# Optimization experiments

Hardware: AMD Instinct MI355X
Metric: run time of the kernel (lower is better)

## Reference

```python
import jax, jax.numpy as jnp
import numpy as np

EPS = 1e-5

def _inorm(x, gamma=None, beta=None):
    # InstanceNorm1d: normalize over last (length) axis per (batch, channel)
    mu = jnp.mean(x, axis=-1, keepdims=True)
    var = jnp.mean(jnp.square(x - mu), axis=-1, keepdims=True)
    y = (x - mu) * jax.lax.rsqrt(var + EPS)
    if gamma is not None:
        y = y * gamma[None, :, None] + beta[None, :, None]
    return y

def _conv1x1(w, x):
    # Conv1d kernel-size-1, bias=False -> channel GEMM
    return jnp.einsum('oi,bin->bon', w, x)

def _channel_attn(Q, K, V, scale):
    scores = jnp.einsum('bin,bjn->bij', Q, K) * scale  # [B, qc, kc]
    attn = jax.nn.softmax(_inorm(scores), axis=-1)
    return jnp.einsum('bij,bjn->bin', attn, V)


def setup_inputs() -> dict:
    key = jax.random.key(0)
    ks = jax.random.split(key, 12)
    C, EC, NC, N = 256, 256, 2, 16384
    H = W = 128
    twoB = 8
    s = C ** -0.5
    return {
        'features': jax.random.normal(ks[0], (twoB, C, H, W), jnp.float32),
        'kv_queue': jax.random.normal(ks[1], (NC, EC, N), jnp.float32) * 0.01,
        'w_in': jax.random.normal(ks[2], (EC, C), jnp.float32) * s,
        'w_out': jax.random.normal(ks[3], (C, EC), jnp.float32) * s,
        'wq_sa': jax.random.normal(ks[4], (EC, EC), jnp.float32) * s,
        'wk_sa': jax.random.normal(ks[5], (EC, EC), jnp.float32) * s,
        'wv_sa': jax.random.normal(ks[6], (EC, EC), jnp.float32) * s,
        'wo_sa': jax.random.normal(ks[7], (EC, EC), jnp.float32) * s,
        'wq_ca': jax.random.normal(ks[8], (EC, EC), jnp.float32) * s,
        'wo_ca': jax.random.normal(ks[9], (EC, EC), jnp.float32) * s,
        'attn_gamma': jnp.ones((EC,), jnp.float32),
        'attn_beta': jnp.zeros((EC,), jnp.float32),
        'enc_gamma': jnp.ones((EC,), jnp.float32),
        'enc_beta': jnp.zeros((EC,), jnp.float32),
    }


def reference(features, kv_queue, w_in, w_out, wq_sa, wk_sa, wv_sa, wo_sa,
              wq_ca, wo_ca, attn_gamma, attn_beta, enc_gamma, enc_beta):
    twoB, C, H, W = features.shape
    B = twoB // 2
    N = H * W
    scale = N ** -0.5
    x = features.reshape(twoB, C, N)
    # map_in: 1x1 conv + exact GELU
    emb = jax.nn.gelu(_conv1x1(w_in, x), approximate=False)
    emb_l, emb_u = emb[:B], emb[B:]
    norm = _inorm(emb, attn_gamma, attn_beta)  # per-sample, safe to batch both halves
    norm_l, norm_u = norm[:B], norm[B:]
    # --- self-attention on unlabeled half (channel-wise) ---
    Qu = _conv1x1(wq_sa, norm_u)
    Ku = _conv1x1(wk_sa, norm_u)
    Vu = _conv1x1(wv_sa, norm_u)
    sa_u = _conv1x1(wo_sa, _channel_attn(Qu, Ku, Vu, scale)) + emb_u
    # --- cross-attention: labeled queries vs semantic-memory queue ---
    Ql = _conv1x1(wq_ca, norm_l)  # [B, ec, N]
    nc, ec, Nq = kv_queue.shape
    kv = kv_queue.reshape(nc * ec, Nq)  # [num_class*ec, N], shared across batch
    scores = jnp.einsum('bin,jn->bij', Ql, kv) * scale  # [B, ec, nc*ec]
    attn = jax.nn.softmax(_inorm(scores), axis=-1)
    ca = jnp.einsum('bij,jn->bin', attn, kv)
    ca_l = _conv1x1(wo_ca, ca) + emb_l
    # --- map_out on enc-normed halves ---
    out_l = jax.nn.gelu(_conv1x1(w_out, _inorm(ca_l, enc_gamma, enc_beta)), approximate=False)
    out_u = jax.nn.gelu(_conv1x1(w_out, _inorm(sa_u, enc_gamma, enc_beta)), approximate=False)
    out = jnp.concatenate([out_l, out_u], axis=0)
    return out.reshape(twoB, C, H, W)
```

## Files before the change

### kernel.cpp

```cpp
#include <hip/hip_runtime.h>
#include <hip/hip_bf16.h>

#define N_DIM 16384
#define CN (256L * 16384)
#define NT_Q 8
#define NT_KCH (N_DIM / NT_Q)

using bf16 = __hip_bfloat16;

typedef __attribute__((ext_vector_type(8))) short short8;
typedef __attribute__((ext_vector_type(4))) float f32x4;
typedef __attribute__((ext_vector_type(4))) unsigned int u32x4;


__device__ __forceinline__ unsigned short f2bf(float x) {
    unsigned int u = __float_as_uint(x);
    u = (u + 0x7FFFu + ((u >> 16) & 1u)) >> 16;
    return (unsigned short)u;
}
__device__ __forceinline__ float bfus2f(unsigned short h) {
    return __uint_as_float(((unsigned int)h) << 16);
}

__device__ __forceinline__ void mfma16(f32x4& d, short8 a, short8 b) {
    asm("v_mfma_f32_16x16x32_bf16 %0, %1, %2, %0" : "+v"(d) : "v"(a), "v"(b));
}

__device__ inline float ldmix(const void* p, long i, int isbf) {
    return isbf ? __bfloat162float(((const bf16*)p)[i])
                : ((const float*)p)[i];
}

__device__ inline void st_out(float* p, long i, float v)  { p[i] = v; }
__device__ inline void st_out(bf16* p, long i, float v)   { p[i] = __float2bfloat16(v); }

__device__ inline float gelu_f(float x) {
    return 0.5f * x * (1.0f + erff(x * 0.70710678118654752440f));
}

__device__ inline float block_reduce_sum(float v, float* sh) {
    int t = threadIdx.x;
    sh[t] = v; __syncthreads();
    for (int s = 128; s >= 1; s >>= 1) {
        if (t < s) sh[t] += sh[t + s];
        __syncthreads();
    }
    float r = sh[0]; __syncthreads();
    return r;
}

__device__ inline float block_reduce_max(float v, float* sh) {
    int t = threadIdx.x;
    sh[t] = v; __syncthreads();
    for (int s = 128; s >= 1; s >>= 1) {
        if (t < s) sh[t] = fmaxf(sh[t], sh[t + s]);
        __syncthreads();
    }
    float r = sh[0]; __syncthreads();
    return r;
}

__device__ __forceinline__ void wr16(short* d, const u32x4* r, int isbf) {
    if (isbf) {
        *(u32x4*)d = r[0]; *(u32x4*)(d + 8) = r[1];
    } else {
        #pragma unroll
        for (int g = 0; g < 2; ++g) {
            short8 h;
            #pragma unroll
            for (int i = 0; i < 8; ++i)
                h[i] = (short)f2bf(__uint_as_float(r[2*g + (i >> 2)][i & 3]));
            *(short8*)(d + g * 8) = h;
        }
    }
}


__global__ void detect_main(const unsigned short* __restrict__ p, int* __restrict__ flag) {
    __shared__ int cnt;
    int t = threadIdx.x;
    if (t == 0) cnt = 0;
    __syncthreads();
    int e = (p[t] >> 7) & 0xFF;
    if (e >= 90 && e <= 145) atomicAdd(&cnt, 1);
    __syncthreads();
    if (t == 0) *flag = (cnt >= 200) ? 1 : 0;
}

__global__ void detect_const(const unsigned short* __restrict__ p, int* __restrict__ flag) {
    __shared__ int zc;
    int t = threadIdx.x;
    if (t == 0) zc = 0;
    __syncthreads();
    if (p[t] == 0) atomicAdd(&zc, 1);
    __syncthreads();
    if (t == 0) *flag = (zc >= 64) ? 0 : 1;
}

__global__ void init_consts(int* flags) {
    flags[2] = 0;
    flags[3] = 1;
}

__global__ void cvt_small(const void* __restrict__ in, float* __restrict__ out,
                          int n, const int* __restrict__ flag) {
    int i = threadIdx.x;
    if (i < n) out[i] = ldmix(in, i, *flag);
}

__global__ void rowsum_kv(const void* __restrict__ kv, float* __restrict__ kvsum,
                          const int* __restrict__ flag) {
    __shared__ float sh[256];
    int j = blockIdx.x, t = threadIdx.x, isbf = *flag;
    float s = 0.f;
    if (isbf) {
        const short8* p = (const short8*)((const bf16*)kv + (long)j * N_DIM);
        for (int i = t; i < N_DIM / 8; i += 256) {
            short8 v = p[i];
            #pragma unroll
            for (int e = 0; e < 8; ++e) s += bfus2f((unsigned short)v[e]);
        }
    } else {
        const float4* p = (const float4*)((const float*)kv + (long)j * N_DIM);
        for (int i = t; i < N_DIM / 4; i += 256) {
            float4 v = p[i];
            s += v.x + v.y + v.z + v.w;
        }
    }
    s = block_reduce_sum(s, sh);
    if (t == 0) kvsum[j] = s;
}

__global__ void row_stats(const bf16* __restrict__ Z,
                          const float* __restrict__ gamma,
                          const float* __restrict__ beta,
                          float4* __restrict__ st) {
    __shared__ float sh[256];
    int row = blockIdx.x, z = blockIdx.y, t = threadIdx.x;
    const short8* zp = (const short8*)(Z + (long)z * CN + (long)row * N_DIM);
    float s = 0.f, s2 = 0.f;
    for (int i = t; i < N_DIM / 8; i += 256) {
        short8 v = zp[i];
        #pragma unroll
        for (int e = 0; e < 8; ++e) {
            float x = bfus2f((unsigned short)v[e]);
            s += x; s2 += x * x;
        }
    }
    float sum  = block_reduce_sum(s, sh);
    float sum2 = block_reduce_sum(s2, sh);
    if (t == 0) {
        float mean = sum * (1.0f / N_DIM);
        float var  = fmaxf(sum2 * (1.0f / N_DIM) - mean * mean, 0.0f);
        float inv  = rsqrtf(var + 1e-5f);
        float sc = gamma[row] * inv;
        st[z * 256 + row] = make_float4(sc, beta[row] - mean * sc, mean, 0.0f);
    }
}

__global__ void inorm_softmax(float* __restrict__ S, int L) {
    __shared__ float sh[256];
    float* row = S + (long)blockIdx.x * L;
    int t = threadIdx.x;
    float x0 = row[t];
    float x1 = (L > 256) ? row[t + 256] : 0.0f;
    float sum = block_reduce_sum(x0 + x1, sh);
    float mean = sum / (float)L;
    float d0 = x0 - mean;
    float d1 = (L > 256) ? (x1 - mean) : 0.0f;
    float var = fmaxf(block_reduce_sum(d0 * d0 + d1 * d1, sh) / (float)L, 0.0f);
    float inv = rsqrtf(var + 1e-5f);
    float y0 = d0 * inv, y1 = d1 * inv;
    float mx = (L > 256) ? fmaxf(y0, y1) : y0;
    float gmax = block_reduce_max(mx, sh);
    float e0 = expf(y0 - gmax);
    float e1 = (L > 256) ? expf(y1 - gmax) : 0.0f;
    float es = block_reduce_sum(e0 + e1, sh);
    float rinv = 1.0f / es;
    row[t] = e0 * rinv;
    if (L > 256) row[t + 256] = e1 * rinv;
}

template <bool RES, bool GELU, typename TOUT>
__global__ __launch_bounds__(256) void gemm_nn_mfma(
    const void* __restrict__ Ag, const int* __restrict__ fA, long astr,
    const void* __restrict__ Bg, const int* __restrict__ fB, long bbase, long bstr,
    const float* __restrict__ rowc, int rstr,
    const bf16* __restrict__ Dres, long dstr,
    TOUT* __restrict__ Cout, long cstr, int K)
{
    __shared__ short Ahi[2][128 * 40];
    __shared__ short Alo[2][128 * 40];
    __shared__ short Bsm[2][32 * 130];

    int t = threadIdx.x;
    int af = *fA, bfg = *fB;
    int z = blockIdx.z;
    int n0 = blockIdx.x * 128, m0 = blockIdx.y * 128;
    int wave = t >> 6, lane = t & 63;
    int wr = wave >> 1, wc = wave & 1;
    int l15 = lane & 15, lkg = lane >> 4;
    int arow = t & 127, ah2 = t >> 7;

    long abase = (long)z * astr;
    long bz = bbase + (long)z * bstr;

    u32x4 ra[4], rb[4];
    f32x4 acc[4][4];
    f32x4 zz = {0.f, 0.f, 0.f, 0.f};
    #pragma unroll
    for (int mi = 0; mi < 4; ++mi)
        #pragma unroll
        for (int ni = 0; ni < 4; ++ni) acc[mi][ni] = zz;

    auto STAGE_LOAD = [&](int k0) {
        long ga = abase + (long)(m0 + arow) * K + k0 + ah2 * 16;
        if (af) {
            const u32x4* p = (const u32x4*)((const unsigned short*)Ag + ga);
            ra[0] = p[0]; ra[1] = p[1];
        } else {
            const u32x4* p = (const u32x4*)((const float*)Ag + ga);
            ra[0] = p[0]; ra[1] = p[1]; ra[2] = p[2]; ra[3] = p[3];
        }
        #pragma unroll
        for (int c = 0; c < 2; ++c) {
            int q = c * 256 + t;
            int k = q >> 4, n = (q & 15) * 8;
            long gb = bz + (long)(k0 + k) * N_DIM + n0 + n;
            if (bfg) {
                rb[c * 2] = *(const u32x4*)((const unsigned short*)Bg + gb);
            } else {
                const u32x4* p = (const u32x4*)((const float*)Bg + gb);
                rb[c * 2] = p[0]; rb[c * 2 + 1] = p[1];
            }
        }
    };

    auto STAGE_WRITE = [&](int b2) {
        short* dh = &Ahi[b2][arow * 40 + ah2 * 16];
        short* dl = &Alo[b2][arow * 40 + ah2 * 16];
        if (af) {
            *(u32x4*)dh = ra[0]; *(u32x4*)(dh + 8) = ra[1];
            u32x4 z4 = {0u, 0u, 0u, 0u};
            *(u32x4*)dl = z4; *(u32x4*)(dl + 8) = z4;
        } else {
            #pragma unroll
            for (int g = 0; g < 2; ++g) {
                short8 h, l;
                #pragma unroll
                for (int i = 0; i < 8; ++i) {
                    float x = __uint_as_float(ra[2 * g + (i >> 2)][i & 3]);
                    unsigned short hu = f2bf(x);
                    h[i] = (short)hu;
                    l[i] = (short)f2bf(x - bfus2f(hu));
                }
                *(short8*)(dh + g * 8) = h;
                *(short8*)(dl + g * 8) = l;
            }
        }
        #pragma unroll
        for (int c = 0; c < 2; ++c) {
            int q = c * 256 + t;
            int k = q >> 4, n = (q & 15) * 8;
            unsigned int* wp = (unsigned int*)&Bsm[b2][k * 130 + n];
            if (bfg) {
                const unsigned int* s = (const unsigned int*)&rb[c * 2];
                wp[0] = s[0]; wp[1] = s[1]; wp[2] = s[2]; wp[3] = s[3];
            } else {
                #pragma unroll
                for (int j = 0; j < 4; ++j) {
                    float x0 = __uint_as_float(rb[c * 2 + (j >> 1)][(j & 1) * 2]);
                    float x1 = __uint_as_float(rb[c * 2 + (j >> 1)][(j & 1) * 2 + 1]);
                    wp[j] = (unsigned int)f2bf(x0) | ((unsigned int)f2bf(x1) << 16);
                }
            }
        }
    };

    auto COMPUTE = [&](int b2) {
        const short* AhB = &Ahi[b2][0];
        const short* AlB = &Alo[b2][0];
        const short* BsB = &Bsm[b2][0];
        short8 bfr[4];
        #pragma unroll
        for (int ni = 0; ni < 4; ++ni) {
            short8 v;
            #pragma unroll
            for (int e = 0; e < 8; ++e)
                v[e] = BsB[(lkg * 8 + e) * 130 + wc * 64 + ni * 16 + l15];
            bfr[ni] = v;
        }
        short8 ahf[4], alf[4];
        #pragma unroll
        for (int mi = 0; mi < 4; ++mi) {
            int ro = (wr * 64 + mi * 16 + l15) * 40 + lkg * 8;
            ahf[mi] = *(const short8*)(AhB + ro);
            alf[mi] = *(const short8*)(AlB + ro);
        }
        #pragma unroll
        for (int mi = 0; mi < 4; ++mi)
            #pragma unroll
            for (int ni = 0; ni < 4; ++ni)
                mfma16(acc[mi][ni], ahf[mi], bfr[ni]);
        #pragma unroll
        for (int mi = 0; mi < 4; ++mi)
            #pragma unroll
            for (int ni = 0; ni < 4; ++ni)
                mfma16(acc[mi][ni], alf[mi], bfr[ni]);
    };

    int nsteps = K >> 5;
    STAGE_LOAD(0);
    STAGE_WRITE(0);
    __syncthreads();
    int buf = 0;
    for (int s = 0; s < nsteps; ++s) {
        bool pre = (s + 1 < nsteps);
        if (pre) STAGE_LOAD((s + 1) << 5);
        COMPUTE(buf);
        if (pre) STAGE_WRITE(buf ^ 1);
        __syncthreads();
        buf ^= 1;
    }

    long cz = (long)z * cstr;
    long dz = (long)z * dstr;
    #pragma unroll
    for (int mi = 0; mi < 4; ++mi) {
        #pragma unroll
        for (int ni = 0; ni < 4; ++ni) {
            int mbase = m0 + wr * 64 + mi * 16 + lkg * 4;
            int n = n0 + wc * 64 + ni * 16 + l15;
            #pragma unroll
            for (int r = 0; r < 4; ++r) {
                int m = mbase + r;
                float v = acc[mi][ni][r];
                if (rowc) v += rowc[z * rstr + m];
                if (RES)  v += __bfloat162float(Dres[dz + (long)m * N_DIM + n]);
                if (GELU) v = gelu_f(v);
                st_out(Cout, cz + (long)m * N_DIM + n, v);
            }
        }
    }
}

__global__ __launch_bounds__(256) void gemm_nt_mfma(
    const void* __restrict__ Ag, const int* __restrict__ fA, long astr,
    const void* __restrict__ Bg, const int* __restrict__ fB, long bstr,
    float* __restrict__ Pout, int J)
{
    __shared__ short Ash[2][128 * 40];
    __shared__ short Bs2[2][128 * 40];

    int t = threadIdx.x;
    int af = *fA, bfg = *fB;
    int zq = blockIdx.z;
    int zb = zq >> 3, q = zq & 7;
    int j0 = blockIdx.x * 128, m0 = blockIdx.y * 128;
    int kz = q * NT_KCH;
    int wave = t >> 6, lane = t & 63;
    int wr = wave >> 1, wc = wave & 1;
    int l15 = lane & 15, lkg = lane >> 4;
    int arow = t & 127, ah2 = t >> 7;

    long abase = (long)zb * astr;
    long bbase = (long)zb * bstr;

    u32x4 ra[4], rbn[4];
    f32x4 acc[4][4];
    f32x4 zz = {0.f, 0.f, 0.f, 0.f};
    #pragma unroll
    for (int mi = 0; mi < 4; ++mi)
        #pragma unroll
        for (int nj = 0; nj < 4; ++nj) acc[mi][nj] = zz;

    auto STAGE_LOAD = [&](int k0) {
        long ga = abase + (long)(m0 + arow) * N_DIM + k0 + ah2 * 16;
        if (af) {
            const u32x4* p = (const u32x4*)((const unsigned short*)Ag + ga);
            ra[0] = p[0]; ra[1] = p[1];
        } else {
            const u32x4* p = (const u32x4*)((const float*)Ag + ga);
            ra[0] = p[0]; ra[1] = p[1]; ra[2] = p[2]; ra[3] = p[3];
        }
        long gb = bbase + (long)(j0 + arow) * N_DIM + k0 + ah2 * 16;
        if (bfg) {
            const u32x4* p = (const u32x4*)((const unsigned short*)Bg + gb);
            rbn[0] = p[0]; rbn[1] = p[1];
        } else {
            const u32x4* p = (const u32x4*)((const float*)Bg + gb);
            rbn[0] = p[0]; rbn[1] = p[1]; rbn[2] = p[2]; rbn[3] = p[3];
        }
    };

    auto STAGE_WRITE = [&](int b2) {
        wr16(&Ash[b2][arow * 40 + ah2 * 16], ra, af);
        wr16(&Bs2[b2][arow * 40 + ah2 * 16], rbn, bfg);
    };

    auto COMPUTE = [&](int b2) {
        const short* AsB = &Ash[b2][0];
        const short* BsB = &Bs2[b2][0];
        short8 a[4], b[4];
        #pragma unroll
        for (int mi = 0; mi < 4; ++mi)
            a[mi] = *(const short8*)(AsB + (wr * 64 + mi * 16 + l15) * 40 + lkg * 8);
        #pragma unroll
        for (int nj = 0; nj < 4; ++nj)
            b[nj] = *(const short8*)(BsB + (wc * 64 + nj * 16 + l15) * 40 + lkg * 8);
        #pragma unroll
        for (int mi = 0; mi < 4; ++mi)
            #pragma unroll
            for (int nj = 0; nj < 4; ++nj)
                mfma16(acc[mi][nj], a[mi], b[nj]);
    };

    int nsteps = NT_KCH >> 5;
    STAGE_LOAD(kz);
    STAGE_WRITE(0);
    __syncthreads();
    int buf = 0;
    for (int s = 0; s < nsteps; ++s) {
        bool pre = (s + 1 < nsteps);
        if (pre) STAGE_LOAD(kz + ((s + 1) << 5));
        COMPUTE(buf);
        if (pre) STAGE_WRITE(buf ^ 1);
        __syncthreads();
        buf ^= 1;
    }

    float* P = Pout + (long)zq * 256 * J;
    #pragma unroll
    for (int mi = 0; mi < 4; ++mi) {
        #pragma unroll
        for (int nj = 0; nj < 4; ++nj) {
            int mbase = m0 + wr * 64 + mi * 16 + lkg * 4;
            int j = j0 + wc * 64 + nj * 16 + l15;
            #pragma unroll
            for (int r = 0; r < 4; ++r)
                P[(long)(mbase + r) * J + j] = acc[mi][nj][r];
        }
    }
}

template <bool TRANSB>
__global__ __launch_bounds__(256) void gemm_small(
    const void* __restrict__ A, const int* __restrict__ fA, int K, long astr,
    const void* __restrict__ B, const int* __restrict__ fB, int ldb, long bstr,
    float* __restrict__ C, int Nn, long cstr, float alpha)
{
    __shared__ float As[64][65];
    __shared__ float Bs[64][65];
    int af = *fA, bfg = *fB;
    int z = blockIdx.z;
    int j0 = blockIdx.x * 64, m0 = blockIdx.y * 64;
    int t = threadIdx.x, tx = t & 15, ty = t >> 4;
    long ab = (long)z * astr, bb = (long)z * bstr;
    float acc[4][4] = {{0.f}};

    for (int k0 = 0; k0 < K; k0 += 64) {
        #pragma unroll
        for (int i = 0; i < 16; ++i) {
            int idx = t + i * 256;
            int r = idx >> 6, c = idx & 63;
            As[c][r] = ldmix(A, ab + (long)(m0 + r) * K + (k0 + c), af);
            if (TRANSB)
                Bs[c][r] = ldmix(B, bb + (long)(j0 + r) * ldb + (k0 + c), bfg);
            else
                Bs[r][c] = ldmix(B, bb + (long)(k0 + r) * ldb + (j0 + c), bfg);
        }
        __syncthreads();
        #pragma unroll
        for (int kk = 0; kk < 64; ++kk) {
            float a[4], bbv[4];
            #pragma unroll
            for (int i = 0; i < 4; ++i) a[i] = As[kk][ty * 4 + i];
            #pragma unroll
            for (int j = 0; j < 4; ++j) bbv[j] = Bs[kk][tx * 4 + j];
            #pragma unroll
            for (int i = 0; i < 4; ++i)
                #pragma unroll
                for (int j = 0; j < 4; ++j)
                    acc[i][j] = fmaf(a[i], bbv[j], acc[i][j]);
        }
        __syncthreads();
    }

    #pragma unroll
    for (int i = 0; i < 4; ++i) {
        int m = m0 + ty * 4 + i;
        #pragma unroll
        for (int j = 0; j < 4; ++j)
            C[(long)z * cstr + (long)m * Nn + (j0 + tx * 4 + j)] = acc[i][j] * alpha;
    }
}


__global__ void build_G(const float* __restrict__ PART, const float4* __restrict__ st,
                        float* __restrict__ G) {
    int z = blockIdx.y, c = blockIdx.x, d = threadIdx.x;
    float g = 0.f;
    for (int q = 0; q < NT_Q; ++q)
        g += PART[((long)(z * NT_Q + q)) * 65536 + c * 256 + d];
    float4 a = st[z * 256 + c], b = st[z * 256 + d];
    float rc = a.z * (float)N_DIM, rd = b.z * (float)N_DIM;
    G[(long)z * 65536 + c * 256 + d] = a.x * b.x * g
                   + a.x * b.y * rc + a.y * b.x * rd
                   + (float)N_DIM * a.y * b.y;
}

__global__ void build_P(const float* __restrict__ PART, const float4* __restrict__ st,
                        const float* __restrict__ kvsum, float* __restrict__ P) {
    int z = blockIdx.y, c = blockIdx.x, t = threadIdx.x;
    float4 a = st[z * 256 + c];
    for (int j = t; j < 512; j += 256) {
        float s = 0.f;
        for (int q = 0; q < NT_Q; ++q)
            s += PART[((long)(z * NT_Q + q)) * 131072 + c * 512 + j];
        P[(long)z * 131072 + c * 512 + j] = a.x * s + a.y * kvsum[j];
    }
}

__global__ void build_Ms_u(const float* __restrict__ M, const float4* __restrict__ st,
                           float* __restrict__ Ms, float* __restrict__ u) {
    __shared__ float sh[256];
    int z = blockIdx.y, m = blockIdx.x, c = threadIdx.x;
    float mv = M[(long)z * 65536 + m * 256 + c];
    float4 b = st[z * 256 + c];
    Ms[(long)z * 65536 + m * 256 + c] = mv * b.x + ((m == c) ? 1.0f : 0.0f);
    float uu = block_reduce_sum(mv * b.y, sh);
    if (c == 0) u[z * 256 + m] = uu;
}

__global__ void build_W2_v(const void* __restrict__ Wout, const int* __restrict__ fM,
                           const float4* __restrict__ st,
                           float* __restrict__ W2, float* __restrict__ v) {
    __shared__ float sh[256];
    int z = blockIdx.y, o = blockIdx.x, c = threadIdx.x;
    float wv = ldmix(Wout, (long)o * 256 + c, *fM);
    float4 b = st[z * 256 + c];
    W2[(long)z * 65536 + o * 256 + c] = wv * b.x;
    float vv = block_reduce_sum(wv * b.y, sh);
    if (c == 0) v[z * 256 + o] = vv;
}

extern "C" void kernel_launch(void* const* d_in, const int* in_sizes, int n_in,
                              void* d_out, int out_size, void* d_ws, size_t ws_size,
                              hipStream_t stream) {
    const void* feats = d_in[0];
    const void* kv    = d_in[1];
    const void* W_in  = d_in[2];
    const void* W_out = d_in[3];
    const void* Wq_sa = d_in[4];
    const void* Wk_sa = d_in[5];
    const void* Wv_sa = d_in[6];
    const void* Wo_sa = d_in[7];
    const void* Wq_ca = d_in[8];
    const void* Wo_ca = d_in[9];
    float* OUT = (float*)d_out;

    char* w = (char*)d_ws;
    auto alloc = [&](size_t bytes) { char* p = w; w += (bytes + 255) & ~255UL; return p; };
    int*    flags = (int*)alloc(64);
    float*  GA    = (float*)alloc(1024);
    float*  GAb   = (float*)alloc(1024);
    float*  EG    = (float*)alloc(1024);
    float*  EGb   = (float*)alloc(1024);
    float*  kvsum = (float*)alloc(2048);
    float4* ST1   = (float4*)alloc(8 * 256 * 16);
    float4* ST2   = (float4*)alloc(8 * 256 * 16);
    float*  Gf4   = (float*)alloc(4L * 65536 * 4);
    float*  T1_4  = (float*)alloc(4L * 65536 * 4);
    float*  T2_4  = (float*)alloc(4L * 65536 * 4);
    float*  Mm4   = (float*)alloc(4L * 65536 * 4);
    float*  Ms4   = (float*)alloc(4L * 65536 * 4);
    float*  W2_8  = (float*)alloc(8L * 65536 * 4);
    float*  SC4   = (float*)alloc(4L * 65536 * 4);
    float*  SCL4  = (float*)alloc(4L * 131072 * 4);
    float*  Pm4   = (float*)alloc(4L * 131072 * 4);
    float*  M2_4  = (float*)alloc(4L * 131072 * 4);
    float*  uvec  = (float*)alloc(4 * 256 * 4);
    float*  vvec  = (float*)alloc(8 * 256 * 4);
    float*  PART  = (float*)alloc(32L * 131072 * 4);
    bf16*   EMB8  = (bf16*)alloc(8 * CN * 2);
    bf16*   SU8   = (bf16*)alloc(8 * CN * 2);

    const int* fM = flags + 0;
    const int* f0 = flags + 2;
    const int* f1 = flags + 3;
    const float scale = 1.0f / 128.0f;

    detect_main<<<1, 256, 0, stream>>>((const unsigned short*)feats, flags + 0);
    detect_const<<<1, 256, 0, stream>>>((const unsigned short*)d_in[10], flags + 1);
    init_consts<<<1, 1, 0, stream>>>(flags);
    cvt_small<<<1, 256, 0, stream>>>(d_in[10], GA,  256, flags + 1);
    cvt_small<<<1, 256, 0, stream>>>(d_in[11], GAb, 256, flags + 1);
    cvt_small<<<1, 256, 0, stream>>>(d_in[12], EG,  256, flags + 1);
    cvt_small<<<1, 256, 0, stream>>>(d_in[13], EGb, 256, flags + 1);
    rowsum_kv<<<512, 256, 0, stream>>>(kv, kvsum, fM);

    gemm_nn_mfma<false, true, bf16><<<dim3(128, 2, 8), 256, 0, stream>>>(
        W_in, fM, 0, feats, fM, 0, CN, nullptr, 0, nullptr, 0, EMB8, CN, 256);
    row_stats<<<dim3(256, 8), 256, 0, stream>>>(EMB8, GA, GAb, ST1);

    gemm_nt_mfma<<<dim3(2, 2, 32), 256, 0, stream>>>(
        EMB8 + 4 * CN, f1, CN, EMB8 + 4 * CN, f1, CN, PART, 256);
    build_G<<<dim3(256, 4), 256, 0, stream>>>(PART, ST1 + 4 * 256, Gf4);
    gemm_small<false><<<dim3(4, 4, 4), 256, 0, stream>>>(
        Wq_sa, fM, 256, 0, Gf4, f0, 256, 65536, T1_4, 256, 65536, 1.0f);
    gemm_small<true><<<dim3(4, 4, 4), 256, 0, stream>>>(
        T1_4, f0, 256, 65536, Wk_sa, fM, 256, 0, SC4, 256, 65536, scale);
    inorm_softmax<<<1024, 256, 0, stream>>>(SC4, 256);
    gemm_small<false><<<dim3(4, 4, 4), 256, 0, stream>>>(
        Wo_sa, fM, 256, 0, SC4, f0, 256, 65536, T2_4, 256, 65536, 1.0f);
    gemm_small<false><<<dim3(4, 4, 4), 256, 0, stream>>>(
        T2_4, f0, 256, 65536, Wv_sa, fM, 256, 0, Mm4, 256, 65536, 1.0f);
    build_Ms_u<<<dim3(256, 4), 256, 0, stream>>>(Mm4, ST1 + 4 * 256, Ms4, uvec);
    gemm_nn_mfma<false, false, bf16><<<dim3(128, 2, 4), 256, 0, stream>>>(
        Ms4, f0, 65536, EMB8, f1, 4 * CN, CN, uvec, 256, nullptr, 0, SU8 + 4 * CN, CN, 256);

    gemm_nt_mfma<<<dim3(4, 2, 32), 256, 0, stream>>>(
        EMB8, f1, CN, kv, fM, 0, PART, 512);
    build_P<<<dim3(256, 4), 256, 0, stream>>>(PART, ST1, kvsum, Pm4);
    gemm_small<false><<<dim3(8, 4, 4), 256, 0, stream>>>(
        Wq_ca, fM, 256, 0, Pm4, f0, 512, 131072, SCL4, 512, 131072, scale);
    inorm_softmax<<<1024, 256, 0, stream>>>(SCL4, 512);
    gemm_small<false><<<dim3(8, 4, 4), 256, 0, stream>>>(
        Wo_ca, fM, 256, 0, SCL4, f0, 512, 131072, M2_4, 512, 131072, 1.0f);
    gemm_nn_mfma<true, false, bf16><<<dim3(128, 2, 4), 256, 0, stream>>>(
        M2_4, f0, 131072, kv, fM, 0, 0, nullptr, 0, EMB8, CN, SU8, CN, 512);

    row_stats<<<dim3(256, 8), 256, 0, stream>>>(SU8, EG, EGb, ST2);
    build_W2_v<<<dim3(256, 8), 256, 0, stream>>>(W_out, fM, ST2, W2_8, vvec);
    gemm_nn_mfma<false, true, float><<<dim3(128, 2, 8), 256, 0, stream>>>(
        W2_8, f0, 65536, SU8, f1, 0, CN, vvec, 256, nullptr, 0, OUT, CN, 256);
}
```

Before: 1.458 ms.

## Transpose B tile into K-contiguous LDS layout and skip lo-MFMA for bf16 A

The B operand is now loaded as strided column pairs and transposed while being written to LDS, so each MFMA B fragment becomes a single vector read instead of eight scalar LDS reads. When A is already bf16, the kernel no longer zero-fills the low-part A buffer and skips the second MFMA pass that previously multiplied by zeros. The cost is that B global loads become narrower and strided across rows (4-byte or 8-byte per row), which may hurt coalescing.

Result: no change. 1.476 ms (+1.2%).

```diff
diff --git a/kernel.cpp b/kernel.cpp
--- a/kernel.cpp
+++ b/kernel.cpp
@@ -191,7 +191,7 @@
 {
     __shared__ short Ahi[2][128 * 40];
     __shared__ short Alo[2][128 * 40];
-    __shared__ short Bsm[2][32 * 130];
+    __shared__ short Bt [2][128 * 40];
 
     int t = threadIdx.x;
     int af = *fA, bfg = *fB;
@@ -201,11 +201,13 @@
     int wr = wave >> 1, wc = wave & 1;
     int l15 = lane & 15, lkg = lane >> 4;
     int arow = t & 127, ah2 = t >> 7;
+    int kq = t & 7, npl = t >> 3;
 
     long abase = (long)z * astr;
     long bz = bbase + (long)z * bstr;
 
-    u32x4 ra[4], rb[4];
+    u32x4 ra[4];
+    unsigned int rb[2][8];
     f32x4 acc[4][4];
     f32x4 zz = {0.f, 0.f, 0.f, 0.f};
     #pragma unroll
@@ -224,26 +226,30 @@
         }
         #pragma unroll
         for (int c = 0; c < 2; ++c) {
-            int q = c * 256 + t;
-            int k = q >> 4, n = (q & 15) * 8;
-            long gb = bz + (long)(k0 + k) * N_DIM + n0 + n;
+            int np = npl + 32 * c;
+            long gb = bz + (long)(k0 + 4 * kq) * N_DIM + n0 + 2 * np;
             if (bfg) {
-                rb[c * 2] = *(const u32x4*)((const unsigned short*)Bg + gb);
+                const unsigned int* p = (const unsigned int*)((const unsigned short*)Bg + gb);
+                #pragma unroll
+                for (int e = 0; e < 4; ++e)
+                    rb[c][e] = p[(long)e * (N_DIM / 2)];
             } else {
-                const u32x4* p = (const u32x4*)((const float*)Bg + gb);
-                rb[c * 2] = p[0]; rb[c * 2 + 1] = p[1];
+                const float* p = (const float*)Bg + gb;
+                #pragma unroll
+                for (int e = 0; e < 4; ++e) {
+                    uint2 v = *(const uint2*)(p + (long)e * N_DIM);
+                    rb[c][2 * e] = v.x; rb[c][2 * e + 1] = v.y;
+                }
             }
         }
     };
 
     auto STAGE_WRITE = [&](int b2) {
         short* dh = &Ahi[b2][arow * 40 + ah2 * 16];
-        short* dl = &Alo[b2][arow * 40 + ah2 * 16];
         if (af) {
             *(u32x4*)dh = ra[0]; *(u32x4*)(dh + 8) = ra[1];
-            u32x4 z4 = {0u, 0u, 0u, 0u};
-            *(u32x4*)dl = z4; *(u32x4*)(dl + 8) = z4;
         } else {
+            short* dl = &Alo[b2][arow * 40 + ah2 * 16];
             #pragma unroll
             for (int g = 0; g < 2; ++g) {
                 short8 h, l;
@@ -260,53 +266,49 @@
         }
         #pragma unroll
         for (int c = 0; c < 2; ++c) {
-            int q = c * 256 + t;
-            int k = q >> 4, n = (q & 15) * 8;
-            unsigned int* wp = (unsigned int*)&Bsm[b2][k * 130 + n];
+            int np = npl + 32 * c;
+            unsigned int w0x, w0y, w1x, w1y;
             if (bfg) {
-                const unsigned int* s = (const unsigned int*)&rb[c * 2];
-                wp[0] = s[0]; wp[1] = s[1]; wp[2] = s[2]; wp[3] = s[3];
+                w0x = (rb[c][0] & 0xFFFFu) | (rb[c][1] << 16);
+                w0y = (rb[c][2] & 0xFFFFu) | (rb[c][3] << 16);
+                w1x = (rb[c][0] >> 16) | (rb[c][1] & 0xFFFF0000u);
+                w1y = (rb[c][2] >> 16) | (rb[c][3] & 0xFFFF0000u);
             } else {
-                #pragma unroll
-                for (int j = 0; j < 4; ++j) {
-                    float x0 = __uint_as_float(rb[c * 2 + (j >> 1)][(j & 1) * 2]);
-                    float x1 = __uint_as_float(rb[c * 2 + (j >> 1)][(j & 1) * 2 + 1]);
-                    wp[j] = (unsigned int)f2bf(x0) | ((unsigned int)f2bf(x1) << 16);
-                }
+                w0x = (unsigned)f2bf(__uint_as_float(rb[c][0])) | ((unsigned)f2bf(__uint_as_float(rb[c][2])) << 16);
+                w0y = (unsigned)f2bf(__uint_as_float(rb[c][4])) | ((unsigned)f2bf(__uint_as_float(rb[c][6])) << 16);
+                w1x = (unsigned)f2bf(__uint_as_float(rb[c][1])) | ((unsigned)f2bf(__uint_as_float(rb[c][3])) << 16);
+                w1y = (unsigned)f2bf(__uint_as_float(rb[c][5])) | ((unsigned)f2bf(__uint_as_float(rb[c][7])) << 16);
             }
+            int n = 2 * np;
+            *(uint2*)&Bt[b2][n * 40 + kq * 4]       = make_uint2(w0x, w0y);
+            *(uint2*)&Bt[b2][(n + 1) * 40 + kq * 4] = make_uint2(w1x, w1y);
         }
     };
 
     auto COMPUTE = [&](int b2) {
-        const short* AhB = &Ahi[b2][0];
-        const short* AlB = &Alo[b2][0];
-        const short* BsB = &Bsm[b2][0];
-        short8 bfr[4];
-        #pragma unroll
-        for (int ni = 0; ni < 4; ++ni) {
-            short8 v;
-            #pragma unroll
-            for (int e = 0; e < 8; ++e)
-                v[e] = BsB[(lkg * 8 + e) * 130 + wc * 64 + ni * 16 + l15];
-            bfr[ni] = v;
-        }
-        short8 ahf[4], alf[4];
-        #pragma unroll
-        for (int mi = 0; mi < 4; ++mi) {
-            int ro = (wr * 64 + mi * 16 + l15) * 40 + lkg * 8;
-            ahf[mi] = *(const short8*)(AhB + ro);
-            alf[mi] = *(const short8*)(AlB + ro);
-        }
+        short8 bfr[4], ahf[4];
+        #pragma unroll
+        for (int ni = 0; ni < 4; ++ni)
+            bfr[ni] = *(const short8*)(&Bt[b2][(wc * 64 + ni * 16 + l15) * 40 + lkg * 8]);
+        #pragma unroll
+        for (int mi = 0; mi < 4; ++mi)
+            ahf[mi] = *(const short8*)(&Ahi[b2][(wr * 64 + mi * 16 + l15) * 40 + lkg * 8]);
         #pragma unroll
         for (int mi = 0; mi < 4; ++mi)
             #pragma unroll
             for (int ni = 0; ni < 4; ++ni)
                 mfma16(acc[mi][ni], ahf[mi], bfr[ni]);
-        #pragma unroll
-        for (int mi = 0; mi < 4; ++mi)
-            #pragma unroll
-            for (int ni = 0; ni < 4; ++ni)
-                mfma16(acc[mi][ni], alf[mi], bfr[ni]);
+        if (!af) {
+            short8 alf[4];
+            #pragma unroll
+            for (int mi = 0; mi < 4; ++mi)
+                alf[mi] = *(const short8*)(&Alo[b2][(wr * 64 + mi * 16 + l15) * 40 + lkg * 8]);
+            #pragma unroll
+            for (int mi = 0; mi < 4; ++mi)
+                #pragma unroll
+                for (int ni = 0; ni < 4; ++ni)
+                    mfma16(acc[mi][ni], alf[mi], bfr[ni]);
+        }
     };
 
     int nsteps = K >> 5;
```
